# Optimization experiments

Measured on AMD Instinct MI355X. Metric: run time of the kernel, lower is better.

The kernel has to match this reference:

```python
import jax, jax.numpy as jnp
import numpy as np

USER_SIZE = 1_000_000
ITEM_SIZE = 1_000_000
EMBED = 64
BATCH = 4096
NUM_TOTAL = 100
STD = 0.01


def setup_inputs() -> dict:
    key = jax.random.key(0)
    ks = jax.random.split(key, 16)
    d = {}
    d["user"] = jax.random.randint(ks[0], (BATCH, 1), 0, USER_SIZE, dtype=jnp.int64 if jax.config.jax_enable_x64 else jnp.int32)
    d["item"] = jax.random.randint(ks[1], (BATCH, NUM_TOTAL), 0, ITEM_SIZE, dtype=jnp.int64 if jax.config.jax_enable_x64 else jnp.int32)
    d["num_total"] = NUM_TOTAL
    # Embedding tables stored as [vocab, embed] (transpose of nn.Linear weight [embed, vocab])
    d["Wu_gmf"] = jax.random.normal(ks[2], (USER_SIZE, EMBED), jnp.float32) * STD
    d["bu_gmf"] = jnp.zeros((EMBED,), jnp.float32)
    d["Wu_mlp"] = jax.random.normal(ks[3], (USER_SIZE, EMBED), jnp.float32) * STD
    d["bu_mlp"] = jnp.zeros((EMBED,), jnp.float32)
    d["Wi_gmf"] = jax.random.normal(ks[4], (ITEM_SIZE, EMBED), jnp.float32) * STD
    d["bi_gmf"] = jnp.zeros((EMBED,), jnp.float32)
    d["Wi_mlp"] = jax.random.normal(ks[5], (ITEM_SIZE, EMBED), jnp.float32) * STD
    d["bi_mlp"] = jnp.zeros((EMBED,), jnp.float32)
    # MLP tower, stored as [in, out]
    d["W1"] = jax.random.normal(ks[6], (2 * EMBED, 2 * EMBED), jnp.float32) * STD
    d["b1"] = jnp.zeros((2 * EMBED,), jnp.float32)
    d["W2"] = jax.random.normal(ks[7], (2 * EMBED, EMBED), jnp.float32) * STD
    d["b2"] = jnp.zeros((EMBED,), jnp.float32)
    d["W3"] = jax.random.normal(ks[8], (EMBED, EMBED // 2), jnp.float32) * STD
    d["b3"] = jnp.zeros((EMBED // 2,), jnp.float32)
    d["Wp"] = jax.random.normal(ks[9], (3 * EMBED // 2, 1), jnp.float32) * STD
    d["bp"] = jnp.zeros((1,), jnp.float32)
    return d


def reference(user, item, num_total, Wu_gmf, bu_gmf, Wu_mlp, bu_mlp, Wi_gmf, bi_gmf, Wi_mlp, bi_mlp, W1, b1, W2, b2, W3, b3, Wp, bp):
    # one-hot @ Linear == embedding gather (column select of weight) + bias
    eu_g = Wu_gmf[user[:, 0]] + bu_gmf              # [B, E]
    eu_m = Wu_mlp[user[:, 0]] + bu_mlp              # [B, E]
    ei_g = Wi_gmf[item] + bi_gmf                    # [B, N, E]
    ei_m = Wi_mlp[item] + bi_mlp                    # [B, N, E]

    gmf = eu_g[:, None, :] * ei_g                   # [B, N, E]

    eu_m_b = jnp.broadcast_to(eu_m[:, None, :], ei_m.shape)
    inter = jnp.concatenate([eu_m_b, ei_m], axis=2)  # [B, N, 2E]
    h1 = jax.nn.relu(inter @ W1 + b1)
    h2 = jax.nn.relu(h1 @ W2 + b2)
    h3 = jax.nn.relu(h2 @ W3 + b3)                  # [B, N, E/2]

    concat = jnp.concatenate([gmf, h3], axis=2)     # [B, N, 3E/2]
    pred = jax.nn.sigmoid(concat @ Wp + bp)         # [B, N, 1]
    return pred[..., 0]                             # [B, N]
```

## Files before the change

kernel.cpp:

```cpp
#include <hip/hip_runtime.h>


typedef __attribute__((ext_vector_type(8))) short bf16x8;
typedef __attribute__((ext_vector_type(4))) float f32x4;

__device__ __forceinline__ short f2bf(float x){
  unsigned u = __float_as_uint(x);
  u += 0x7fffu + ((u >> 16) & 1u);
  return (short)(u >> 16);
}
__device__ __forceinline__ unsigned char f2fp8(float x){
  return (unsigned char)(__builtin_amdgcn_cvt_pk_fp8_f32(x, 0.f, 0, false) & 0xFF);
}


__global__ __launch_bounds__(256) void ncf_prep_w(
    const float* __restrict__ W1, const float* __restrict__ W2,
    const float* __restrict__ W3, const float* __restrict__ b1,
    const float* __restrict__ bi_mlp, char* __restrict__ ws)
{
  if (blockIdx.x == 104){
    int j = threadIdx.x;
    if (j < 128){
      float acc = b1[j];
      #pragma unroll 4
      for (int k = 0; k < 64; k++)
        acc += bi_mlp[k] * W1[(64 + k)*128 + j];
      ((float*)(ws + 34816))[j] = acc;
    }
    return;
  }
  int i = blockIdx.x * 256 + threadIdx.x;
  if (i < 8192){
    int col = i >> 6, k = i & 63;
    ((short*)ws)[i] = f2bf(W1[k*128 + col]);
  } else if (i < 16384){
    int t = i - 8192; int col = t >> 6, k = t & 63;
    ((unsigned char*)(ws + 16384))[t] = f2fp8(W1[(64 + k)*128 + col]);
  } else if (i < 24576){
    int t = i - 16384; int col = t >> 7, k = t & 127;
    ((unsigned char*)(ws + 24576))[t] = f2fp8(W2[k*64 + col]);
  } else {
    int t = i - 24576; int col = t >> 6, k = t & 63;
    ((unsigned char*)(ws + 32768))[t] = f2fp8(W3[k*32 + col]);
  }
}

__global__ __launch_bounds__(256) void ncf_prep_u(
    const int* __restrict__ user,
    const float* __restrict__ Wu_gmf, const float* __restrict__ bu_gmf,
    const float* __restrict__ Wu_mlp, const float* __restrict__ bu_mlp,
    const float* __restrict__ bi_gmf, const float* __restrict__ Wp,
    const short* __restrict__ W1uT, const float* __restrict__ c1,
    float* __restrict__ Xu, float* __restrict__ wup, float* __restrict__ cu)
{
  __shared__ __align__(16) short s_eu[64][72];
  const int tid = threadIdx.x;
  const int r = tid >> 2, q = tid & 3;
  const int b = blockIdx.x * 64 + r;
  long u = (long)user[b];
  {
    const float4* ump = (const float4*)(Wu_mlp + u*64) + q*4;
    const float4* bmp = (const float4*)(bu_mlp) + q*4;
    const float4* ugp = (const float4*)(Wu_gmf + u*64) + q*4;
    const float4* bgp = (const float4*)(bu_gmf) + q*4;
    const float4* wpp = (const float4*)(Wp) + q*4;
    const float4* bip = (const float4*)(bi_gmf) + q*4;
    float4* wdst = (float4*)(wup + (long)b*64) + q*4;
    bf16x8 ea[2];
    float cacc = 0.f;
    #pragma unroll
    for (int j = 0; j < 4; j++){
      float4 m = ump[j], mb = bmp[j];
      int h = j >> 1, s = (j & 1) * 4;
      ea[h][s+0] = f2bf(m.x + mb.x); ea[h][s+1] = f2bf(m.y + mb.y);
      ea[h][s+2] = f2bf(m.z + mb.z); ea[h][s+3] = f2bf(m.w + mb.w);
      float4 g = ugp[j], gb = bgp[j], wp = wpp[j], bi = bip[j];
      float4 wg; wg.x = (g.x+gb.x)*wp.x; wg.y = (g.y+gb.y)*wp.y;
                 wg.z = (g.z+gb.z)*wp.z; wg.w = (g.w+gb.w)*wp.w;
      wdst[j] = wg;
      cacc += wg.x*bi.x + wg.y*bi.y + wg.z*bi.z + wg.w*bi.w;
    }
    *(bf16x8*)&s_eu[r][q*16]     = ea[0];
    *(bf16x8*)&s_eu[r][q*16 + 8] = ea[1];
    cacc += __shfl_xor(cacc, 1);
    cacc += __shfl_xor(cacc, 2);
    if (q == 0) cu[b] = cacc;
  }
  __syncthreads();

  const int w = tid >> 6, l = tid & 63, lr = l & 15, lg = l >> 4;
  f32x4 acc[4][2];
  #pragma unroll
  for (int mt = 0; mt < 4; mt++)
    #pragma unroll
    for (int nt = 0; nt < 2; nt++)
      acc[mt][nt] = (f32x4){0.f, 0.f, 0.f, 0.f};
  #pragma unroll
  for (int ks = 0; ks < 2; ks++){
    bf16x8 af[4];
    #pragma unroll
    for (int mt = 0; mt < 4; mt++)
      af[mt] = *(const bf16x8*)&s_eu[mt*16 + lr][ks*32 + lg*8];
    #pragma unroll
    for (int nt = 0; nt < 2; nt++){
      bf16x8 bf_ = *(const bf16x8*)&W1uT[(w*32 + nt*16 + lr)*64 + ks*32 + lg*8];
      #pragma unroll
      for (int mt = 0; mt < 4; mt++)
        acc[mt][nt] = __builtin_amdgcn_mfma_f32_16x16x32_bf16(af[mt], bf_, acc[mt][nt], 0, 0, 0);
    }
  }
  #pragma unroll
  for (int nt = 0; nt < 2; nt++){
    int col = w*32 + nt*16 + lr;
    float cc = c1[col];
    #pragma unroll
    for (int mt = 0; mt < 4; mt++)
      #pragma unroll
      for (int rr = 0; rr < 4; rr++){
        int row = mt*16 + lg*4 + rr;
        Xu[(long)(blockIdx.x*64 + row)*128 + col] = acc[mt][nt][rr] + cc;
      }
  }
}

__global__ __launch_bounds__(256, 6) void ncf_main(
    const int* __restrict__ item,
    const float* __restrict__ Wi_mlp, const float* __restrict__ Wi_gmf,
    const unsigned char* __restrict__ W1iT, const unsigned char* __restrict__ W2T,
    const unsigned char* __restrict__ W3T,
    const float* __restrict__ b2, const float* __restrict__ b3,
    const float* __restrict__ Wp, const float* __restrict__ bp,
    const float* __restrict__ Xu, const float* __restrict__ wup,
    const float* __restrict__ cu,
    float* __restrict__ out, int N, int total, int Bsz)
{
  __shared__ __align__(16) unsigned char s_item[64][80];
  __shared__ __align__(16) unsigned char s_h1[64][136];
  __shared__ __align__(16) unsigned char s_h2[64][80];
  __shared__ __align__(16) float s_xu[2][128];
  __shared__            float s_pg[64];

  const int tid = threadIdx.x;
  const int p0  = blockIdx.x * 64;
  const int b0  = p0 / N;
  const int thr = (b0 + 1) * N;
  const int r   = tid >> 2, q = tid & 3;
  const int w   = tid >> 6, l = tid & 63;
  const int lr  = l & 15,  lg = l >> 4;
  const float bp0 = bp[0];

  {
    int p = p0 + r;
    int b = b0 + ((p >= thr) ? 1 : 0);
    long ib = (long)item[p] * 64;
    const float4* mp = (const float4*)(Wi_mlp + ib) + q*4;
    const float4* gp = (const float4*)(Wi_gmf + ib) + q*4;
    const float4* wq = (const float4*)(wup + (long)b*64) + q*4;
    float pg = 0.f;
    int pk[4];
    #pragma unroll
    for (int j = 0; j < 4; j++){
      float4 m = mp[j], g = gp[j], wv = wq[j];
      pg += g.x*wv.x + g.y*wv.y + g.z*wv.z + g.w*wv.w;
      int t_ = __builtin_amdgcn_cvt_pk_fp8_f32(m.x, m.y, 0, false);
      t_     = __builtin_amdgcn_cvt_pk_fp8_f32(m.z, m.w, t_, true);
      pk[j] = t_;
    }
    *(int4*)&s_item[r][q*16] = (int4){pk[0], pk[1], pk[2], pk[3]};
    pg += __shfl_xor(pg, 1);
    pg += __shfl_xor(pg, 2);
    if (q == 0) s_pg[r] = pg + cu[b];
    int i2 = tid >> 7, col = tid & 127;
    int bb = b0 + i2; if (bb >= Bsz) bb = Bsz - 1;
    s_xu[i2][col] = Xu[(long)bb*128 + col];
  }
  __syncthreads();

  #pragma unroll
  for (int mt = 0; mt < 2; mt++){
    f32x4 acc[4];
    #pragma unroll
    for (int nt = 0; nt < 4; nt++) acc[nt] = (f32x4){0.f, 0.f, 0.f, 0.f};
    #pragma unroll
    for (int ks = 0; ks < 2; ks++){
      long af = *(const long*)&W1iT[((w*2 + mt)*16 + lr)*64 + ks*32 + lg*8];
      #pragma unroll
      for (int nt = 0; nt < 4; nt++){
        long bf_ = *(const long*)&s_item[nt*16 + lr][ks*32 + lg*8];
        acc[nt] = __builtin_amdgcn_mfma_f32_16x16x32_fp8_fp8(af, bf_, acc[nt], 0, 0, 0);
      }
    }
    int colb = (w*2 + mt)*16 + lg*4;
    #pragma unroll
    for (int nt = 0; nt < 4; nt++){
      int pair = nt*16 + lr;
      int bl = (p0 + pair >= thr) ? 1 : 0;
      float4 xv = *(const float4*)&s_xu[bl][colb];
      float v0 = acc[nt][0] + xv.x; v0 = v0 > 0.f ? v0 : 0.f;
      float v1 = acc[nt][1] + xv.y; v1 = v1 > 0.f ? v1 : 0.f;
      float v2 = acc[nt][2] + xv.z; v2 = v2 > 0.f ? v2 : 0.f;
      float v3 = acc[nt][3] + xv.w; v3 = v3 > 0.f ? v3 : 0.f;
      int t_ = __builtin_amdgcn_cvt_pk_fp8_f32(v0, v1, 0, false);
      t_     = __builtin_amdgcn_cvt_pk_fp8_f32(v2, v3, t_, true);
      *(int*)&s_h1[pair][colb] = t_;
    }
  }
  __syncthreads();

  {
    f32x4 acc[4];
    #pragma unroll
    for (int nt = 0; nt < 4; nt++) acc[nt] = (f32x4){0.f, 0.f, 0.f, 0.f};
    #pragma unroll
    for (int ks = 0; ks < 4; ks++){
      long af = *(const long*)&W2T[(w*16 + lr)*128 + ks*32 + lg*8];
      #pragma unroll
      for (int nt = 0; nt < 4; nt++){
        long bf_ = *(const long*)&s_h1[nt*16 + lr][ks*32 + lg*8];
        acc[nt] = __builtin_amdgcn_mfma_f32_16x16x32_fp8_fp8(af, bf_, acc[nt], 0, 0, 0);
      }
    }
    int colb = w*16 + lg*4;
    float4 b2v = *(const float4*)&b2[colb];
    #pragma unroll
    for (int nt = 0; nt < 4; nt++){
      int pair = nt*16 + lr;
      float v0 = acc[nt][0] + b2v.x; v0 = v0 > 0.f ? v0 : 0.f;
      float v1 = acc[nt][1] + b2v.y; v1 = v1 > 0.f ? v1 : 0.f;
      float v2 = acc[nt][2] + b2v.z; v2 = v2 > 0.f ? v2 : 0.f;
      float v3 = acc[nt][3] + b2v.w; v3 = v3 > 0.f ? v3 : 0.f;
      int t_ = __builtin_amdgcn_cvt_pk_fp8_f32(v0, v1, 0, false);
      t_     = __builtin_amdgcn_cvt_pk_fp8_f32(v2, v3, t_, true);
      *(int*)&s_h2[pair][colb] = t_;
    }
  }
  __syncthreads();

  {
    f32x4 acc[2];
    #pragma unroll
    for (int mt = 0; mt < 2; mt++) acc[mt] = (f32x4){0.f, 0.f, 0.f, 0.f};
    #pragma unroll
    for (int ks = 0; ks < 2; ks++){
      long bf_ = *(const long*)&s_h2[w*16 + lr][ks*32 + lg*8];
      #pragma unroll
      for (int mt = 0; mt < 2; mt++){
        long af = *(const long*)&W3T[(mt*16 + lr)*64 + ks*32 + lg*8];
        acc[mt] = __builtin_amdgcn_mfma_f32_16x16x32_fp8_fp8(af, bf_, acc[mt], 0, 0, 0);
      }
    }
    float t = 0.f;
    #pragma unroll
    for (int mt = 0; mt < 2; mt++){
      int colb = mt*16 + lg*4;
      float4 b3v = *(const float4*)&b3[colb];
      float4 wpv = *(const float4*)&Wp[64 + colb];
      float v0 = acc[mt][0] + b3v.x; v0 = v0 > 0.f ? v0 : 0.f;
      float v1 = acc[mt][1] + b3v.y; v1 = v1 > 0.f ? v1 : 0.f;
      float v2 = acc[mt][2] + b3v.z; v2 = v2 > 0.f ? v2 : 0.f;
      float v3 = acc[mt][3] + b3v.w; v3 = v3 > 0.f ? v3 : 0.f;
      t += v0*wpv.x + v1*wpv.y + v2*wpv.z + v3*wpv.w;
    }
    t += __shfl_xor(t, 16);
    t += __shfl_xor(t, 32);
    if (l < 16){
      int pair = w*16 + l;
      int p = p0 + pair;
      if (p < total){
        float z = t + s_pg[pair] + bp0;
        out[p] = 1.f / (1.f + __expf(-z));
      }
    }
  }
}

extern "C" void kernel_launch(void* const* d_in, const int* in_sizes, int n_in,
                              void* d_out, int out_size, void* d_ws, size_t ws_size,
                              hipStream_t stream)
{
  const int*   user   = (const int*)  d_in[0];
  const int*   item   = (const int*)  d_in[1];
  const float* Wu_gmf = (const float*)d_in[3];
  const float* bu_gmf = (const float*)d_in[4];
  const float* Wu_mlp = (const float*)d_in[5];
  const float* bu_mlp = (const float*)d_in[6];
  const float* Wi_gmf = (const float*)d_in[7];
  const float* bi_gmf = (const float*)d_in[8];
  const float* Wi_mlp = (const float*)d_in[9];
  const float* bi_mlp = (const float*)d_in[10];
  const float* W1     = (const float*)d_in[11];
  const float* b1     = (const float*)d_in[12];
  const float* W2     = (const float*)d_in[13];
  const float* b2     = (const float*)d_in[14];
  const float* W3     = (const float*)d_in[15];
  const float* b3     = (const float*)d_in[16];
  const float* Wp     = (const float*)d_in[17];
  const float* bp     = (const float*)d_in[18];

  int B     = in_sizes[0];
  int total = in_sizes[1];
  int N     = total / B;

  char* wsb = (char*)d_ws;
  short*         W1uT = (short*)wsb;
  unsigned char* W1iT = (unsigned char*)(wsb + 16384);
  unsigned char* W2T  = (unsigned char*)(wsb + 24576);
  unsigned char* W3T  = (unsigned char*)(wsb + 32768);
  float*         c1   = (float*)(wsb + 34816);
  float*         Xu   = (float*)(wsb + 36864);
  float*         wup  = Xu  + (size_t)B * 128;
  float*         cuv  = wup + (size_t)B * 64;

  ncf_prep_w<<<105, 256, 0, stream>>>(W1, W2, W3, b1, bi_mlp, wsb);
  ncf_prep_u<<<B/64, 256, 0, stream>>>(user, Wu_gmf, bu_gmf, Wu_mlp, bu_mlp,
                                       bi_gmf, Wp, W1uT, c1, Xu, wup, cuv);

  int nblk = (total + 63) / 64;
  ncf_main<<<nblk, 256, 0, stream>>>(item, Wi_mlp, Wi_gmf,
      W1iT, W2T, W3T, b2, b3, Wp, bp, Xu, wup, cuv,
      (float*)d_out, N, total, B);
}
```

Measured before the change: 70.22 us.

## Merge weight and user prep into one launch with scalar fp32 user projection

Replaces the two prep kernels with a single launch: one 128-thread block per user computes the user-side W1 projection in plain fp32 scalar FMA (dropping the bf16 MFMA path and the separate c1 bias vector), while extra blocks quantize W1-item, W2 and W3 to fp8. This removes a kernel launch and the serial dependency between weight prep and user prep, and avoids bf16 rounding of the user projection. In exchange the user projection is no longer on matrix cores; each block rereads W1 column-wise through cache and uses 4096 small blocks.

Result: slower. 72.14 us (+2.7%).

```diff
diff --git a/kernel.cpp b/kernel.cpp
--- a/kernel.cpp
+++ b/kernel.cpp
@@ -4,123 +4,54 @@
 typedef __attribute__((ext_vector_type(8))) short bf16x8;
 typedef __attribute__((ext_vector_type(4))) float f32x4;
 
-__device__ __forceinline__ short f2bf(float x){
-  unsigned u = __float_as_uint(x);
-  u += 0x7fffu + ((u >> 16) & 1u);
-  return (short)(u >> 16);
-}
 __device__ __forceinline__ unsigned char f2fp8(float x){
   return (unsigned char)(__builtin_amdgcn_cvt_pk_fp8_f32(x, 0.f, 0, false) & 0xFF);
 }
 
 
-__global__ __launch_bounds__(256) void ncf_prep_w(
-    const float* __restrict__ W1, const float* __restrict__ W2,
-    const float* __restrict__ W3, const float* __restrict__ b1,
-    const float* __restrict__ bi_mlp, char* __restrict__ ws)
-{
-  if (blockIdx.x == 104){
-    int j = threadIdx.x;
-    if (j < 128){
-      float acc = b1[j];
-      #pragma unroll 4
-      for (int k = 0; k < 64; k++)
-        acc += bi_mlp[k] * W1[(64 + k)*128 + j];
-      ((float*)(ws + 34816))[j] = acc;
-    }
-    return;
-  }
-  int i = blockIdx.x * 256 + threadIdx.x;
-  if (i < 8192){
-    int col = i >> 6, k = i & 63;
-    ((short*)ws)[i] = f2bf(W1[k*128 + col]);
-  } else if (i < 16384){
-    int t = i - 8192; int col = t >> 6, k = t & 63;
-    ((unsigned char*)(ws + 16384))[t] = f2fp8(W1[(64 + k)*128 + col]);
-  } else if (i < 24576){
-    int t = i - 16384; int col = t >> 7, k = t & 127;
-    ((unsigned char*)(ws + 24576))[t] = f2fp8(W2[k*64 + col]);
-  } else {
-    int t = i - 24576; int col = t >> 6, k = t & 63;
-    ((unsigned char*)(ws + 32768))[t] = f2fp8(W3[k*32 + col]);
-  }
-}
-
-__global__ __launch_bounds__(256) void ncf_prep_u(
+__global__ __launch_bounds__(128) void ncf_prep(
     const int* __restrict__ user,
     const float* __restrict__ Wu_gmf, const float* __restrict__ bu_gmf,
     const float* __restrict__ Wu_mlp, const float* __restrict__ bu_mlp,
-    const float* __restrict__ bi_gmf, const float* __restrict__ Wp,
-    const short* __restrict__ W1uT, const float* __restrict__ c1,
-    float* __restrict__ Xu, float* __restrict__ wup, float* __restrict__ cu)
+    const float* __restrict__ bi_gmf, const float* __restrict__ bi_mlp,
+    const float* __restrict__ W1, const float* __restrict__ b1,
+    const float* __restrict__ W2, const float* __restrict__ W3,
+    const float* __restrict__ Wp,
+    unsigned char* __restrict__ wsT, float* __restrict__ Xu,
+    float* __restrict__ wup, float* __restrict__ cu, int B)
 {
-  __shared__ __align__(16) short s_eu[64][72];
-  const int tid = threadIdx.x;
-  const int r = tid >> 2, q = tid & 3;
-  const int b = blockIdx.x * 64 + r;
-  long u = (long)user[b];
-  {
-    const float4* ump = (const float4*)(Wu_mlp + u*64) + q*4;
-    const float4* bmp = (const float4*)(bu_mlp) + q*4;
-    const float4* ugp = (const float4*)(Wu_gmf + u*64) + q*4;
-    const float4* bgp = (const float4*)(bu_gmf) + q*4;
-    const float4* wpp = (const float4*)(Wp) + q*4;
-    const float4* bip = (const float4*)(bi_gmf) + q*4;
-    float4* wdst = (float4*)(wup + (long)b*64) + q*4;
-    bf16x8 ea[2];
-    float cacc = 0.f;
-    #pragma unroll
-    for (int j = 0; j < 4; j++){
-      float4 m = ump[j], mb = bmp[j];
-      int h = j >> 1, s = (j & 1) * 4;
-      ea[h][s+0] = f2bf(m.x + mb.x); ea[h][s+1] = f2bf(m.y + mb.y);
-      ea[h][s+2] = f2bf(m.z + mb.z); ea[h][s+3] = f2bf(m.w + mb.w);
-      float4 g = ugp[j], gb = bgp[j], wp = wpp[j], bi = bip[j];
-      float4 wg; wg.x = (g.x+gb.x)*wp.x; wg.y = (g.y+gb.y)*wp.y;
-                 wg.z = (g.z+gb.z)*wp.z; wg.w = (g.w+gb.w)*wp.w;
-      wdst[j] = wg;
-      cacc += wg.x*bi.x + wg.y*bi.y + wg.z*bi.z + wg.w*bi.w;
-    }
-    *(bf16x8*)&s_eu[r][q*16]     = ea[0];
-    *(bf16x8*)&s_eu[r][q*16 + 8] = ea[1];
-    cacc += __shfl_xor(cacc, 1);
-    cacc += __shfl_xor(cacc, 2);
-    if (q == 0) cu[b] = cacc;
-  }
-  __syncthreads();
-
-  const int w = tid >> 6, l = tid & 63, lr = l & 15, lg = l >> 4;
-  f32x4 acc[4][2];
-  #pragma unroll
-  for (int mt = 0; mt < 4; mt++)
-    #pragma unroll
-    for (int nt = 0; nt < 2; nt++)
-      acc[mt][nt] = (f32x4){0.f, 0.f, 0.f, 0.f};
-  #pragma unroll
-  for (int ks = 0; ks < 2; ks++){
-    bf16x8 af[4];
-    #pragma unroll
-    for (int mt = 0; mt < 4; mt++)
-      af[mt] = *(const bf16x8*)&s_eu[mt*16 + lr][ks*32 + lg*8];
-    #pragma unroll
-    for (int nt = 0; nt < 2; nt++){
-      bf16x8 bf_ = *(const bf16x8*)&W1uT[(w*32 + nt*16 + lr)*64 + ks*32 + lg*8];
-      #pragma unroll
-      for (int mt = 0; mt < 4; mt++)
-        acc[mt][nt] = __builtin_amdgcn_mfma_f32_16x16x32_bf16(af[mt], bf_, acc[mt][nt], 0, 0, 0);
-    }
-  }
-  #pragma unroll
-  for (int nt = 0; nt < 2; nt++){
-    int col = w*32 + nt*16 + lr;
-    float cc = c1[col];
-    #pragma unroll
-    for (int mt = 0; mt < 4; mt++)
-      #pragma unroll
-      for (int rr = 0; rr < 4; rr++){
-        int row = mt*16 + lg*4 + rr;
-        Xu[(long)(blockIdx.x*64 + row)*128 + col] = acc[mt][nt][rr] + cc;
-      }
+  int bid = blockIdx.x;
+  int j = threadIdx.x;
+  if (bid < B){
+    long u = (long)user[bid];
+    float acc = b1[j];
+    #pragma unroll 4
+    for (int k = 0; k < 64; k++){
+      float eu = Wu_mlp[u*64 + k] + bu_mlp[k];
+      acc += eu * W1[k*128 + j] + bi_mlp[k] * W1[(64 + k)*128 + j];
+    }
+    Xu[(long)bid*128 + j] = acc;
+    if (j < 64){
+      float wg = (Wu_gmf[u*64 + j] + bu_gmf[j]) * Wp[j];
+      wup[(long)bid*64 + j] = wg;
+      float c = wg * bi_gmf[j];
+      c += __shfl_xor(c, 1);  c += __shfl_xor(c, 2);
+      c += __shfl_xor(c, 4);  c += __shfl_xor(c, 8);
+      c += __shfl_xor(c, 16); c += __shfl_xor(c, 32);
+      if (j == 0) cu[bid] = c;
+    }
+    return;
+  }
+  int i = (bid - B)*128 + j;
+  if (i < 8192){
+    int col = i >> 6, k = i & 63;
+    wsT[i] = f2fp8(W1[(64 + k)*128 + col]);
+  } else if (i < 16384){
+    int t = i - 8192; int col = t >> 7, k = t & 127;
+    wsT[i] = f2fp8(W2[k*64 + col]);
+  } else {
+    int t = i - 16384; int col = (t - 0) >> 6, k = t & 63;
+    wsT[i] = f2fp8(W3[k*32 + col]);
   }
 }
 
@@ -303,18 +234,16 @@
   int N     = total / B;
 
   char* wsb = (char*)d_ws;
-  short*         W1uT = (short*)wsb;
-  unsigned char* W1iT = (unsigned char*)(wsb + 16384);
-  unsigned char* W2T  = (unsigned char*)(wsb + 24576);
-  unsigned char* W3T  = (unsigned char*)(wsb + 32768);
-  float*         c1   = (float*)(wsb + 34816);
-  float*         Xu   = (float*)(wsb + 36864);
+  unsigned char* W1iT = (unsigned char*)wsb;
+  unsigned char* W2T  = (unsigned char*)(wsb + 8192);
+  unsigned char* W3T  = (unsigned char*)(wsb + 16384);
+  float*         Xu   = (float*)(wsb + 18432);
   float*         wup  = Xu  + (size_t)B * 128;
   float*         cuv  = wup + (size_t)B * 64;
 
-  ncf_prep_w<<<105, 256, 0, stream>>>(W1, W2, W3, b1, bi_mlp, wsb);
-  ncf_prep_u<<<B/64, 256, 0, stream>>>(user, Wu_gmf, bu_gmf, Wu_mlp, bu_mlp,
-                                       bi_gmf, Wp, W1uT, c1, Xu, wup, cuv);
+  ncf_prep<<<B + 144, 128, 0, stream>>>(user, Wu_gmf, bu_gmf, Wu_mlp, bu_mlp,
+                                        bi_gmf, bi_mlp, W1, b1, W2, W3, Wp,
+                                        (unsigned char*)d_ws, Xu, wup, cuv, B);
 
   int nblk = (total + 63) / 64;
   ncf_main<<<nblk, 256, 0, stream>>>(item, Wi_mlp, Wi_gmf,
```
